# Performance work log

Hardware: AMD Instinct MI355X
Metric: run time of the kernel (lower is better)

The kernel has to match this reference:

```python
import jax, jax.numpy as jnp
import numpy as np

B, IN_UNITS, C, U, K = 32, 16, 8192, 32, 16
NUM_ITERS = 3


def setup_inputs() -> dict:
    key = jax.random.key(0)
    k1, k2 = jax.random.split(key)
    x = jax.random.normal(k1, (B, IN_UNITS, C), dtype=jnp.float32)
    # W corresponds to the torch parameter of shape (1, C, U, K, IN_UNITS), leading 1 dropped
    W = jax.random.normal(k2, (C, U, K, IN_UNITS), dtype=jnp.float32)
    return {"x": x, "W": W}


def reference(x, W):
    batch = x.shape[0]
    # u_hat[b,c,u,k] = sum_i W[c,u,k,i] * x[b,i,c]   (torch: W @ x after transpose/stack)
    u_hat = jnp.einsum('cuki,bic->bcuk', W, x)
    b_ij = jnp.zeros((C, U), dtype=x.dtype)
    v = None
    for _ in range(NUM_ITERS):
        c_ij = jax.nn.softmax(b_ij, axis=0)            # softmax over in_channels (dim=1 in torch)
        s = jnp.einsum('cu,bcuk->buk', c_ij, u_hat)    # weighted sum over channels
        # squash: note the original sums over dim=2 of (B,1,U,K,1) == the num_units axis
        mag_sq = jnp.sum(s ** 2, axis=1, keepdims=True)  # (B,1,K)
        mag = jnp.sqrt(mag_sq)
        v = mag_sq / (1.0 + mag_sq) * (s / mag)          # (B,U,K)
        # agreement: mean over batch of <u_hat, v>
        a = jnp.einsum('bcuk,buk->cu', u_hat, v) / batch
        b_ij = b_ij + a
    return v[..., None]  # matches torch output (B, num_units, unit_size, 1)
```

## Files before the change

kernel.cpp:

```cpp
#include <hip/hip_runtime.h>

#define CC   8192
#define UU   32
#define BB   32
#define INU  16
#define UK   512
#define CPB  32
#define NBLK 256
#define XS_STRIDE 528

template <int CTRL>
__device__ __forceinline__ float dpp_add(float x) {
  int p = __builtin_amdgcn_update_dpp(0, __float_as_int(x), CTRL, 0xF, 0xF, true);
  return x + __int_as_float(p);
}

__global__ __launch_bounds__(512, 2) void fused_pass(
    const float* __restrict__ x, const float* __restrict__ W,
    const float* __restrict__ v_in, float* __restrict__ b_io,
    float* __restrict__ S, float* __restrict__ Z, const int iter0)
{
    __shared__ float xs[16 * XS_STRIDE];

    const int t  = threadIdx.x;
    const int w  = t >> 6;
    const int l  = t & 63;
    const int k  = l & 15;
    const int bg = l >> 4;
    const int u0 = w * 4;
    const int c0 = blockIdx.x * CPB;

    float v[4][8], Sl[4][8];
#pragma unroll
    for (int j = 0; j < 4; ++j)
#pragma unroll
      for (int bb = 0; bb < 8; ++bb) Sl[j][bb] = 0.f;

    if (iter0) {
#pragma unroll
      for (int j = 0; j < 4; ++j)
#pragma unroll
        for (int bb = 0; bb < 8; ++bb) v[j][bb] = 0.f;
    } else {
#pragma unroll
      for (int j = 0; j < 4; ++j)
#pragma unroll
        for (int bb = 0; bb < 8; ++bb)
          v[j][bb] = v_in[(bg * 8 + bb) * UK + (u0 + j) * 16 + k];
    }
    float zloc[4] = {0.f, 0.f, 0.f, 0.f};

    for (int cc = 0; cc < CPB; ++cc) {
        if ((cc & 15) == 0) {
            __syncthreads();
            const int cbase = c0 + (cc & ~15);
#pragma unroll
            for (int jj = 0; jj < 16; ++jj) {
                int idx = jj * 512 + t;
                int ccl = idx & 15;
                int bi  = idx >> 4;
                int b   = bi >> 4, i = bi & 15;
                xs[ccl * XS_STRIDE + (b & 7) * 64 + (b >> 3) * 16 + i] = x[bi * CC + cbase + ccl];
            }
            __syncthreads();
        }

        const int c = c0 + cc;

        float bold[4] = {0.f, 0.f, 0.f, 0.f};
        if (!iter0) {
#pragma unroll
            for (int j = 0; j < 4; ++j) bold[j] = b_io[(size_t)c * UU + u0 + j];
        }

        float4 wq[4][4];
        {
            const float4* wp = (const float4*)(W + ((size_t)c * UK + (size_t)u0 * 16 + k) * INU);
#pragma unroll
            for (int j = 0; j < 4; ++j)
#pragma unroll
                for (int q = 0; q < 4; ++q) wq[j][q] = wp[j * 64 + q];
        }

        float uh[4][8];
        float ap[4] = {0.f, 0.f, 0.f, 0.f};
        const float* xrow = &xs[(cc & 15) * XS_STRIDE + bg * 16];
#pragma unroll
        for (int bb = 0; bb < 8; ++bb) {
            const float4* xr = (const float4*)(xrow + bb * 64);
            float4 x0 = xr[0], x1 = xr[1], x2 = xr[2], x3 = xr[3];
#pragma unroll
            for (int j = 0; j < 4; ++j) {
                float h;
                h = wq[j][0].x * x0.x;
                h = fmaf(wq[j][0].y, x0.y, h); h = fmaf(wq[j][0].z, x0.z, h); h = fmaf(wq[j][0].w, x0.w, h);
                h = fmaf(wq[j][1].x, x1.x, h); h = fmaf(wq[j][1].y, x1.y, h);
                h = fmaf(wq[j][1].z, x1.z, h); h = fmaf(wq[j][1].w, x1.w, h);
                h = fmaf(wq[j][2].x, x2.x, h); h = fmaf(wq[j][2].y, x2.y, h);
                h = fmaf(wq[j][2].z, x2.z, h); h = fmaf(wq[j][2].w, x2.w, h);
                h = fmaf(wq[j][3].x, x3.x, h); h = fmaf(wq[j][3].y, x3.y, h);
                h = fmaf(wq[j][3].z, x3.z, h); h = fmaf(wq[j][3].w, x3.w, h);
                uh[j][bb] = h;
                ap[j] = fmaf(h, v[j][bb], ap[j]);
            }
        }

#pragma unroll
        for (int j = 0; j < 4; ++j) {
            float a = ap[j];
            a = dpp_add<0xB1>(a);
            a = dpp_add<0x4E>(a);
            a = dpp_add<0x141>(a);
            a = dpp_add<0x140>(a);
            a += __shfl_xor(a, 16);
            a += __shfl_xor(a, 32);
            ap[j] = a;
        }

#pragma unroll
        for (int j = 0; j < 4; ++j) {
            float bnew = bold[j] + ap[j] * (1.0f / 32.0f);
            float e = __expf(bnew);
            zloc[j] += e;
            if (l == 0) b_io[(size_t)c * UU + u0 + j] = bnew;
#pragma unroll
            for (int bb = 0; bb < 8; ++bb) Sl[j][bb] = fmaf(e, uh[j][bb], Sl[j][bb]);
        }
    }

#pragma unroll
    for (int j = 0; j < 4; ++j)
#pragma unroll
        for (int bb = 0; bb < 8; ++bb)
            atomicAdd(S + (bg * 8 + bb) * UK + (u0 + j) * 16 + k, Sl[j][bb]);
    if (l == 0) {
#pragma unroll
        for (int j = 0; j < 4; ++j) atomicAdd(Z + u0 + j, zloc[j]);
    }
}

__global__ void squash_k(const float* __restrict__ S, const float* __restrict__ Z,
                         float* __restrict__ vout)
{
    __shared__ float z_sh[UU];
    __shared__ float s2_sh[UK];
    __shared__ float mag_sh[16];

    const int b = blockIdx.x;
    const int t = threadIdx.x;

    if (t < UU) z_sh[t] = Z[t];
    float ssum = S[b * UK + t];
    __syncthreads();

    float s = ssum / z_sh[t >> 4];
    s2_sh[t] = s * s;
    __syncthreads();

    if (t < 16) {
        float m = 0.f;
        for (int uu = 0; uu < UU; ++uu) m += s2_sh[uu * 16 + t];
        mag_sh[t] = m;
    }
    __syncthreads();

    float msq = mag_sh[t & 15];
    float out = (msq / (1.0f + msq)) * s / sqrtf(msq);
    vout[b * UK + t] = out;
}

extern "C" void kernel_launch(void* const* d_in, const int* in_sizes, int n_in,
                              void* d_out, int out_size, void* d_ws, size_t ws_size,
                              hipStream_t stream)
{
    const float* x = (const float*)d_in[0];
    const float* W = (const float*)d_in[1];
    float* out = (float*)d_out;

    char* ws = (char*)d_ws;
    const size_t SLOT = 65536 + 256;
    float* vb  = (float*)(ws + 3 * SLOT);
    float* bio = (float*)(ws + 3 * SLOT + 65536);

    hipMemsetAsync(ws, 0, 3 * SLOT, stream);

    for (int pass = 0; pass < 3; ++pass) {
        float* S = (float*)(ws + pass * SLOT);
        float* Z = (float*)(ws + pass * SLOT + 65536);
        fused_pass<<<NBLK, 512, 0, stream>>>(x, W, vb, bio, S, Z, pass == 0 ? 1 : 0);
        squash_k<<<BB, 512, 0, stream>>>(S, Z, (pass == 2) ? out : vb);
    }
}
```

Baseline: 770.2 us.

## Fuse all routing passes into one cooperative kernel with register-resident logits

Replaces the six launches (three fused passes plus three squash kernels) with a single cooperative kernel that uses grid.sync between passes. Each block recomputes the squash redundantly to get v in registers, and routing logits b stay in registers via readlane instead of a global round trip. Blocks grow to 1024 threads with 2 units per wave, and the channel traversal alternates direction across passes so the most recently loaded W rows may still be cached. The costs are the grid-wide barrier, redundant per-block squash work with shared-memory atomics, and higher register pressure under launch_bounds(1024,4).

```diff
diff --git a/kernel.cpp b/kernel.cpp
--- a/kernel.cpp
+++ b/kernel.cpp
@@ -1,4 +1,7 @@
 #include <hip/hip_runtime.h>
+#include <hip/hip_cooperative_groups.h>
+
+namespace cg = cooperative_groups;
 
 #define CC   8192
 #define UU   32
@@ -7,7 +10,8 @@
 #define UK   512
 #define CPB  32
 #define NBLK 256
-#define XS_STRIDE 528
+#define HALF 16
+#define XSTR 532
 
 template <int CTRL>
 __device__ __forceinline__ float dpp_add(float x) {
@@ -15,179 +19,228 @@
   return x + __int_as_float(p);
 }
 
-__global__ __launch_bounds__(512, 2) void fused_pass(
+__device__ __forceinline__ float red64(float a) {
+  a = dpp_add<0xB1>(a);
+  a = dpp_add<0x4E>(a);
+  a = dpp_add<0x141>(a);
+  a = dpp_add<0x140>(a);
+  a += __shfl_xor(a, 16);
+  a += __shfl_xor(a, 32);
+  return a;
+}
+
+__global__ __launch_bounds__(1024, 4) void caps_all(
     const float* __restrict__ x, const float* __restrict__ W,
-    const float* __restrict__ v_in, float* __restrict__ b_io,
-    float* __restrict__ S, float* __restrict__ Z, const int iter0)
+    float* __restrict__ Sg, float* __restrict__ Zg, float* __restrict__ out)
 {
-    __shared__ float xs[16 * XS_STRIDE];
-
-    const int t  = threadIdx.x;
-    const int w  = t >> 6;
-    const int l  = t & 63;
-    const int k  = l & 15;
-    const int bg = l >> 4;
-    const int u0 = w * 4;
-    const int c0 = blockIdx.x * CPB;
-
-    float v[4][8], Sl[4][8];
-#pragma unroll
-    for (int j = 0; j < 4; ++j)
-#pragma unroll
-      for (int bb = 0; bb < 8; ++bb) Sl[j][bb] = 0.f;
-
-    if (iter0) {
-#pragma unroll
-      for (int j = 0; j < 4; ++j)
-#pragma unroll
-        for (int bb = 0; bb < 8; ++bb) v[j][bb] = 0.f;
-    } else {
-#pragma unroll
-      for (int j = 0; j < 4; ++j)
-#pragma unroll
-        for (int bb = 0; bb < 8; ++bb)
-          v[j][bb] = v_in[(bg * 8 + bb) * UK + (u0 + j) * 16 + k];
+  __shared__ float xs[HALF * XSTR];
+  __shared__ float msq[BB * 16];
+
+  const int t  = threadIdx.x;
+  const int l  = t & 63;
+  const int k  = l & 15;
+  const int bg = l >> 4;
+  const int u0 = (t >> 6) * 2;
+  const int c0 = blockIdx.x * CPB;
+
+  float b0 = 0.f, b1 = 0.f;
+  float v0[8], v1[8];
+#pragma unroll
+  for (int bb = 0; bb < 8; ++bb) { v0[bb] = 0.f; v1[bb] = 0.f; }
+
+  cg::grid_group grid = cg::this_grid();
+
+#pragma unroll 1
+  for (int pass = 0; pass < 3; ++pass) {
+    float* S = Sg + pass * (BB * UK);
+    float* Z = Zg + pass * UU;
+    const int dir = pass & 1;
+
+    float Sl0[8], Sl1[8];
+#pragma unroll
+    for (int bb = 0; bb < 8; ++bb) { Sl0[bb] = 0.f; Sl1[bb] = 0.f; }
+    float z0 = 0.f, z1 = 0.f;
+
+#pragma unroll 1
+    for (int hh = 0; hh < 2; ++hh) {
+      const int h = dir ? (1 - hh) : hh;
+      const int cbase = c0 + h * HALF;
+      __syncthreads();
+#pragma unroll
+      for (int jj = 0; jj < 8; ++jj) {
+        int idx = jj * 1024 + t;
+        int ccl = idx & 15, bi = idx >> 4;
+        int b = bi >> 4, i = bi & 15;
+        xs[ccl * XSTR + (b & 7) * 64 + (b >> 3) * 16 + i] = x[bi * CC + cbase + ccl];
+      }
+      __syncthreads();
+
+#pragma unroll 1
+      for (int ci = 0; ci < HALF; ++ci) {
+        const int ccl = dir ? (HALF - 1 - ci) : ci;
+        const int c   = cbase + ccl;
+        const int cc  = h * HALF + ccl;
+
+        const float4* wp = (const float4*)(W + ((size_t)c * UK + u0 * 16 + k) * INU);
+        float4 wa0 = wp[0],  wa1 = wp[1],  wa2 = wp[2],  wa3 = wp[3];
+        float4 wb0 = wp[64], wb1 = wp[65], wb2 = wp[66], wb3 = wp[67];
+
+        float uh0[8], uh1[8];
+        float ap0 = 0.f, ap1 = 0.f;
+        const float* xr0 = xs + ccl * XSTR + bg * 16;
+#pragma unroll
+        for (int bb = 0; bb < 8; ++bb) {
+          const float4* xr = (const float4*)(xr0 + bb * 64);
+          float4 x0 = xr[0], x1 = xr[1], x2 = xr[2], x3 = xr[3];
+          float h0, h1;
+          h0 = wa0.x * x0.x;
+          h0 = fmaf(wa0.y, x0.y, h0); h0 = fmaf(wa0.z, x0.z, h0); h0 = fmaf(wa0.w, x0.w, h0);
+          h0 = fmaf(wa1.x, x1.x, h0); h0 = fmaf(wa1.y, x1.y, h0);
+          h0 = fmaf(wa1.z, x1.z, h0); h0 = fmaf(wa1.w, x1.w, h0);
+          h0 = fmaf(wa2.x, x2.x, h0); h0 = fmaf(wa2.y, x2.y, h0);
+          h0 = fmaf(wa2.z, x2.z, h0); h0 = fmaf(wa2.w, x2.w, h0);
+          h0 = fmaf(wa3.x, x3.x, h0); h0 = fmaf(wa3.y, x3.y, h0);
+          h0 = fmaf(wa3.z, x3.z, h0); h0 = fmaf(wa3.w, x3.w, h0);
+          h1 = wb0.x * x0.x;
+          h1 = fmaf(wb0.y, x0.y, h1); h1 = fmaf(wb0.z, x0.z, h1); h1 = fmaf(wb0.w, x0.w, h1);
+          h1 = fmaf(wb1.x, x1.x, h1); h1 = fmaf(wb1.y, x1.y, h1);
+          h1 = fmaf(wb1.z, x1.z, h1); h1 = fmaf(wb1.w, x1.w, h1);
+          h1 = fmaf(wb2.x, x2.x, h1); h1 = fmaf(wb2.y, x2.y, h1);
+          h1 = fmaf(wb2.z, x2.z, h1); h1 = fmaf(wb2.w, x2.w, h1);
+          h1 = fmaf(wb3.x, x3.x, h1); h1 = fmaf(wb3.y, x3.y, h1);
+          h1 = fmaf(wb3.z, x3.z, h1); h1 = fmaf(wb3.w, x3.w, h1);
+          uh0[bb] = h0; uh1[bb] = h1;
+          ap0 = fmaf(h0, v0[bb], ap0);
+          ap1 = fmaf(h1, v1[bb], ap1);
+        }
+
+        ap0 = red64(ap0);
+        ap1 = red64(ap1);
+
+        float bo0 = __int_as_float(__builtin_amdgcn_readlane(__float_as_int(b0), cc));
+        float bo1 = __int_as_float(__builtin_amdgcn_readlane(__float_as_int(b1), cc));
+        float bn0 = fmaf(ap0, 0.03125f, bo0);
+        float bn1 = fmaf(ap1, 0.03125f, bo1);
+        b0 = (l == cc) ? bn0 : b0;
+        b1 = (l == cc) ? bn1 : b1;
+        float e0 = __expf(bn0);
+        float e1 = __expf(bn1);
+        z0 += e0; z1 += e1;
+#pragma unroll
+        for (int bb = 0; bb < 8; ++bb) {
+          Sl0[bb] = fmaf(e0, uh0[bb], Sl0[bb]);
+          Sl1[bb] = fmaf(e1, uh1[bb], Sl1[bb]);
+        }
+      }
     }
-    float zloc[4] = {0.f, 0.f, 0.f, 0.f};
-
-    for (int cc = 0; cc < CPB; ++cc) {
-        if ((cc & 15) == 0) {
-            __syncthreads();
-            const int cbase = c0 + (cc & ~15);
-#pragma unroll
-            for (int jj = 0; jj < 16; ++jj) {
-                int idx = jj * 512 + t;
-                int ccl = idx & 15;
-                int bi  = idx >> 4;
-                int b   = bi >> 4, i = bi & 15;
-                xs[ccl * XS_STRIDE + (b & 7) * 64 + (b >> 3) * 16 + i] = x[bi * CC + cbase + ccl];
-            }
-            __syncthreads();
+
+#pragma unroll
+    for (int bb = 0; bb < 8; ++bb) {
+      atomicAdd(S + (bg * 8 + bb) * UK + u0 * 16 + k,       Sl0[bb]);
+      atomicAdd(S + (bg * 8 + bb) * UK + (u0 + 1) * 16 + k, Sl1[bb]);
+    }
+    if (l == 0) { atomicAdd(Z + u0, z0); atomicAdd(Z + u0 + 1, z1); }
+
+    __threadfence();
+    grid.sync();
+
+    if (pass < 2) {
+      if (t < 512) msq[t] = 0.f;
+      __syncthreads();
+      {
+        const int b = t >> 5, uu2 = t & 31;
+        float rz = 1.0f / Z[uu2];
+        const float4* sp = (const float4*)(S + t * 16);
+        float4 s0 = sp[0], s1 = sp[1], s2 = sp[2], s3 = sp[3];
+        float* mrow = msq + b * 16;
+        float q;
+        q = s0.x * rz; atomicAdd(mrow + 0,  q * q);
+        q = s0.y * rz; atomicAdd(mrow + 1,  q * q);
+        q = s0.z * rz; atomicAdd(mrow + 2,  q * q);
+        q = s0.w * rz; atomicAdd(mrow + 3,  q * q);
+        q = s1.x * rz; atomicAdd(mrow + 4,  q * q);
+        q = s1.y * rz; atomicAdd(mrow + 5,  q * q);
+        q = s1.z * rz; atomicAdd(mrow + 6,  q * q);
+        q = s1.w * rz; atomicAdd(mrow + 7,  q * q);
+        q = s2.x * rz; atomicAdd(mrow + 8,  q * q);
+        q = s2.y * rz; atomicAdd(mrow + 9,  q * q);
+        q = s2.z * rz; atomicAdd(mrow + 10, q * q);
+        q = s2.w * rz; atomicAdd(mrow + 11, q * q);
+        q = s3.x * rz; atomicAdd(mrow + 12, q * q);
+        q = s3.y * rz; atomicAdd(mrow + 13, q * q);
+        q = s3.z * rz; atomicAdd(mrow + 14, q * q);
+        q = s3.w * rz; atomicAdd(mrow + 15, q * q);
+      }
+      __syncthreads();
+      {
+        float rz0 = 1.0f / Z[u0], rz1 = 1.0f / Z[u0 + 1];
+#pragma unroll
+        for (int bb = 0; bb < 8; ++bb) {
+          int b = bg * 8 + bb;
+          float m = msq[b * 16 + k];
+          float g = sqrtf(m) / (1.0f + m);
+          v0[bb] = S[b * UK + u0 * 16 + k] * rz0 * g;
+          v1[bb] = S[b * UK + (u0 + 1) * 16 + k] * rz1 * g;
         }
-
-        const int c = c0 + cc;
-
-        float bold[4] = {0.f, 0.f, 0.f, 0.f};
-        if (!iter0) {
-#pragma unroll
-            for (int j = 0; j < 4; ++j) bold[j] = b_io[(size_t)c * UU + u0 + j];
-        }
-
-        float4 wq[4][4];
-        {
-            const float4* wp = (const float4*)(W + ((size_t)c * UK + (size_t)u0 * 16 + k) * INU);
-#pragma unroll
-            for (int j = 0; j < 4; ++j)
-#pragma unroll
-                for (int q = 0; q < 4; ++q) wq[j][q] = wp[j * 64 + q];
-        }
-
-        float uh[4][8];
-        float ap[4] = {0.f, 0.f, 0.f, 0.f};
-        const float* xrow = &xs[(cc & 15) * XS_STRIDE + bg * 16];
-#pragma unroll
-        for (int bb = 0; bb < 8; ++bb) {
-            const float4* xr = (const float4*)(xrow + bb * 64);
-            float4 x0 = xr[0], x1 = xr[1], x2 = xr[2], x3 = xr[3];
-#pragma unroll
-            for (int j = 0; j < 4; ++j) {
-                float h;
-                h = wq[j][0].x * x0.x;
-                h = fmaf(wq[j][0].y, x0.y, h); h = fmaf(wq[j][0].z, x0.z, h); h = fmaf(wq[j][0].w, x0.w, h);
-                h = fmaf(wq[j][1].x, x1.x, h); h = fmaf(wq[j][1].y, x1.y, h);
-                h = fmaf(wq[j][1].z, x1.z, h); h = fmaf(wq[j][1].w, x1.w, h);
-                h = fmaf(wq[j][2].x, x2.x, h); h = fmaf(wq[j][2].y, x2.y, h);
-                h = fmaf(wq[j][2].z, x2.z, h); h = fmaf(wq[j][2].w, x2.w, h);
-                h = fmaf(wq[j][3].x, x3.x, h); h = fmaf(wq[j][3].y, x3.y, h);
-                h = fmaf(wq[j][3].z, x3.z, h); h = fmaf(wq[j][3].w, x3.w, h);
-                uh[j][bb] = h;
-                ap[j] = fmaf(h, v[j][bb], ap[j]);
-            }
-        }
-
-#pragma unroll
-        for (int j = 0; j < 4; ++j) {
-            float a = ap[j];
-            a = dpp_add<0xB1>(a);
-            a = dpp_add<0x4E>(a);
-            a = dpp_add<0x141>(a);
-            a = dpp_add<0x140>(a);
-            a += __shfl_xor(a, 16);
-            a += __shfl_xor(a, 32);
-            ap[j] = a;
-        }
-
-#pragma unroll
-        for (int j = 0; j < 4; ++j) {
-            float bnew = bold[j] + ap[j] * (1.0f / 32.0f);
-            float e = __expf(bnew);
-            zloc[j] += e;
-            if (l == 0) b_io[(size_t)c * UU + u0 + j] = bnew;
-#pragma unroll
-            for (int bb = 0; bb < 8; ++bb) Sl[j][bb] = fmaf(e, uh[j][bb], Sl[j][bb]);
-        }
+      }
+    } else if (blockIdx.x == 0) {
+      if (t < 512) msq[t] = 0.f;
+      __syncthreads();
+      const int b = t >> 5, uu2 = t & 31;
+      float rz = 1.0f / Z[uu2];
+      const float4* sp = (const float4*)(S + t * 16);
+      float4 s0 = sp[0], s1 = sp[1], s2 = sp[2], s3 = sp[3];
+      s0.x *= rz; s0.y *= rz; s0.z *= rz; s0.w *= rz;
+      s1.x *= rz; s1.y *= rz; s1.z *= rz; s1.w *= rz;
+      s2.x *= rz; s2.y *= rz; s2.z *= rz; s2.w *= rz;
+      s3.x *= rz; s3.y *= rz; s3.z *= rz; s3.w *= rz;
+      float* mrow = msq + b * 16;
+      atomicAdd(mrow + 0,  s0.x * s0.x); atomicAdd(mrow + 1,  s0.y * s0.y);
+      atomicAdd(mrow + 2,  s0.z * s0.z); atomicAdd(mrow + 3,  s0.w * s0.w);
+      atomicAdd(mrow + 4,  s1.x * s1.x); atomicAdd(mrow + 5,  s1.y * s1.y);
+      atomicAdd(mrow + 6,  s1.z * s1.z); atomicAdd(mrow + 7,  s1.w * s1.w);
+      atomicAdd(mrow + 8,  s2.x * s2.x); atomicAdd(mrow + 9,  s2.y * s2.y);
+      atomicAdd(mrow + 10, s2.z * s2.z); atomicAdd(mrow + 11, s2.w * s2.w);
+      atomicAdd(mrow + 12, s3.x * s3.x); atomicAdd(mrow + 13, s3.y * s3.y);
+      atomicAdd(mrow + 14, s3.z * s3.z); atomicAdd(mrow + 15, s3.w * s3.w);
+      __syncthreads();
+      float4 o0, o1, o2, o3;
+      o0.x = s0.x * sqrtf(mrow[0])  / (1.0f + mrow[0]);
+      o0.y = s0.y * sqrtf(mrow[1])  / (1.0f + mrow[1]);
+      o0.z = s0.z * sqrtf(mrow[2])  / (1.0f + mrow[2]);
+      o0.w = s0.w * sqrtf(mrow[3])  / (1.0f + mrow[3]);
+      o1.x = s1.x * sqrtf(mrow[4])  / (1.0f + mrow[4]);
+      o1.y = s1.y * sqrtf(mrow[5])  / (1.0f + mrow[5]);
+      o1.z = s1.z * sqrtf(mrow[6])  / (1.0f + mrow[6]);
+      o1.w = s1.w * sqrtf(mrow[7])  / (1.0f + mrow[7]);
+      o2.x = s2.x * sqrtf(mrow[8])  / (1.0f + mrow[8]);
+      o2.y = s2.y * sqrtf(mrow[9])  / (1.0f + mrow[9]);
+      o2.z = s2.z * sqrtf(mrow[10]) / (1.0f + mrow[10]);
+      o2.w = s2.w * sqrtf(mrow[11]) / (1.0f + mrow[11]);
+      o3.x = s3.x * sqrtf(mrow[12]) / (1.0f + mrow[12]);
+      o3.y = s3.y * sqrtf(mrow[13]) / (1.0f + mrow[13]);
+      o3.z = s3.z * sqrtf(mrow[14]) / (1.0f + mrow[14]);
+      o3.w = s3.w * sqrtf(mrow[15]) / (1.0f + mrow[15]);
+      float4* op = (float4*)(out + t * 16);
+      op[0] = o0; op[1] = o1; op[2] = o2; op[3] = o3;
     }
-
-#pragma unroll
-    for (int j = 0; j < 4; ++j)
-#pragma unroll
-        for (int bb = 0; bb < 8; ++bb)
-            atomicAdd(S + (bg * 8 + bb) * UK + (u0 + j) * 16 + k, Sl[j][bb]);
-    if (l == 0) {
-#pragma unroll
-        for (int j = 0; j < 4; ++j) atomicAdd(Z + u0 + j, zloc[j]);
-    }
-}
-
-__global__ void squash_k(const float* __restrict__ S, const float* __restrict__ Z,
-                         float* __restrict__ vout)
-{
-    __shared__ float z_sh[UU];
-    __shared__ float s2_sh[UK];
-    __shared__ float mag_sh[16];
-
-    const int b = blockIdx.x;
-    const int t = threadIdx.x;
-
-    if (t < UU) z_sh[t] = Z[t];
-    float ssum = S[b * UK + t];
-    __syncthreads();
-
-    float s = ssum / z_sh[t >> 4];
-    s2_sh[t] = s * s;
-    __syncthreads();
-
-    if (t < 16) {
-        float m = 0.f;
-        for (int uu = 0; uu < UU; ++uu) m += s2_sh[uu * 16 + t];
-        mag_sh[t] = m;
-    }
-    __syncthreads();
-
-    float msq = mag_sh[t & 15];
-    float out = (msq / (1.0f + msq)) * s / sqrtf(msq);
-    vout[b * UK + t] = out;
+  }
 }
 
 extern "C" void kernel_launch(void* const* d_in, const int* in_sizes, int n_in,
                               void* d_out, int out_size, void* d_ws, size_t ws_size,
                               hipStream_t stream)
 {
-    const float* x = (const float*)d_in[0];
-    const float* W = (const float*)d_in[1];
-    float* out = (float*)d_out;
-
-    char* ws = (char*)d_ws;
-    const size_t SLOT = 65536 + 256;
-    float* vb  = (float*)(ws + 3 * SLOT);
-    float* bio = (float*)(ws + 3 * SLOT + 65536);
-
-    hipMemsetAsync(ws, 0, 3 * SLOT, stream);
-
-    for (int pass = 0; pass < 3; ++pass) {
-        float* S = (float*)(ws + pass * SLOT);
-        float* Z = (float*)(ws + pass * SLOT + 65536);
-        fused_pass<<<NBLK, 512, 0, stream>>>(x, W, vb, bio, S, Z, pass == 0 ? 1 : 0);
-        squash_k<<<BB, 512, 0, stream>>>(S, Z, (pass == 2) ? out : vb);
-    }
-}
+  const float* x = (const float*)d_in[0];
+  const float* W = (const float*)d_in[1];
+  float* out = (float*)d_out;
+
+  float* Sg = (float*)d_ws;
+  float* Zg = (float*)((char*)d_ws + 3 * BB * UK * 4);
+
+  (void)hipMemsetAsync(d_ws, 0, 3 * BB * UK * 4 + 3 * UU * 4, stream);
+
+  void* args[] = { (void*)&x, (void*)&W, (void*)&Sg, (void*)&Zg, (void*)&out };
+  (void)hipLaunchCooperativeKernel(reinterpret_cast<void*>(caps_all),
+                                   dim3(NBLK), dim3(1024), args, 0, stream);
+}
```

New measurement: 1.283 ms. 66.6% more time.

## Fold squash into fused pass, halve chunk size, reverse chunk order per pass

Applied to the files above, without the earlier changes.

Each pass now recomputes the squashed v from the previous pass's S and Z inside every block, which removes two squash kernel launches. CPB drops to 16 with 512 blocks and launch bounds of 4 blocks per SM to raise occupancy. Routing logits are kept in registers and updated with readlane, with one store at the end, and odd passes walk the chunks in reverse so the W and x read last are still in cache. The cost is that every block redundantly reads S_prev and recomputes the magnitudes, and more blocks mean more atomic adds into S.

```diff
diff --git a/kernel.cpp b/kernel.cpp
--- a/kernel.cpp
+++ b/kernel.cpp
@@ -5,9 +5,10 @@
 #define BB   32
 #define INU  16
 #define UK   512
-#define CPB  32
-#define NBLK 256
-#define XS_STRIDE 528
+#define CPB    16
+#define NCHUNK 512
+#define XSTR  532
+#define MSTR  17
 
 template <int CTRL>
 __device__ __forceinline__ float dpp_add(float x) {
@@ -15,179 +16,211 @@
   return x + __int_as_float(p);
 }
 
-__global__ __launch_bounds__(512, 2) void fused_pass(
+__device__ __forceinline__ float red64(float a) {
+  a = dpp_add<0xB1>(a);
+  a = dpp_add<0x4E>(a);
+  a = dpp_add<0x141>(a);
+  a = dpp_add<0x140>(a);
+  a += __shfl_xor(a, 16);
+  a += __shfl_xor(a, 32);
+  return a;
+}
+
+__global__ __launch_bounds__(512, 4) void fused_pass(
     const float* __restrict__ x, const float* __restrict__ W,
-    const float* __restrict__ v_in, float* __restrict__ b_io,
-    float* __restrict__ S, float* __restrict__ Z, const int iter0)
+    float* __restrict__ b_io,
+    const float* __restrict__ S_prev, const float* __restrict__ Z_prev,
+    float* __restrict__ S, float* __restrict__ Z, const int pass)
 {
-    __shared__ float xs[16 * XS_STRIDE];
-
-    const int t  = threadIdx.x;
-    const int w  = t >> 6;
-    const int l  = t & 63;
-    const int k  = l & 15;
-    const int bg = l >> 4;
-    const int u0 = w * 4;
-    const int c0 = blockIdx.x * CPB;
-
-    float v[4][8], Sl[4][8];
+  __shared__ float xs[CPB * XSTR];
+  __shared__ float zr_sh[UU];
+  __shared__ float msq_sh[BB * MSTR];
+
+  const int t  = threadIdx.x;
+  const int l  = t & 63;
+  const int k  = l & 15;
+  const int bg = l >> 4;
+  const int u0 = (t >> 6) * 4;
+  const int dir = pass & 1;
+  const int chunk = dir ? (NCHUNK - 1 - blockIdx.x) : blockIdx.x;
+  const int c0 = chunk * CPB;
+
+  float v[4][8];
+  float breg[4] = {0.f, 0.f, 0.f, 0.f};
+
+  if (pass == 0) {
 #pragma unroll
     for (int j = 0; j < 4; ++j)
 #pragma unroll
-      for (int bb = 0; bb < 8; ++bb) Sl[j][bb] = 0.f;
-
-    if (iter0) {
+      for (int bb = 0; bb < 8; ++bb) v[j][bb] = 0.f;
+  } else {
+#pragma unroll
+    for (int j = 0; j < 4; ++j)
+      breg[j] = b_io[(size_t)(c0 + (l & 15)) * UU + u0 + j];
+
+    if (t < UU) zr_sh[t] = 1.0f / Z_prev[t];
+    __syncthreads();
+    {
+      const int b = t >> 4, k2 = t & 15;
+      float m = 0.f;
+#pragma unroll
+      for (int uu = 0; uu < UU; ++uu) {
+        float s = S_prev[b * UK + uu * 16 + k2] * zr_sh[uu];
+        m = fmaf(s, s, m);
+      }
+      msq_sh[b * MSTR + k2] = m;
+    }
+    __syncthreads();
+    {
+      float zr0 = zr_sh[u0], zr1 = zr_sh[u0 + 1], zr2 = zr_sh[u0 + 2], zr3 = zr_sh[u0 + 3];
+#pragma unroll
+      for (int bb = 0; bb < 8; ++bb) {
+        const int b = bg * 8 + bb;
+        float m = msq_sh[b * MSTR + k];
+        float g = sqrtf(m) / (1.0f + m);
+        v[0][bb] = S_prev[b * UK + (u0 + 0) * 16 + k] * zr0 * g;
+        v[1][bb] = S_prev[b * UK + (u0 + 1) * 16 + k] * zr1 * g;
+        v[2][bb] = S_prev[b * UK + (u0 + 2) * 16 + k] * zr2 * g;
+        v[3][bb] = S_prev[b * UK + (u0 + 3) * 16 + k] * zr3 * g;
+      }
+    }
+    __syncthreads();
+  }
+
+#pragma unroll
+  for (int jj = 0; jj < 16; ++jj) {
+    int idx = jj * 512 + t;
+    int ccl = idx & 15, bi = idx >> 4;
+    int b = bi >> 4, i = bi & 15;
+    xs[ccl * XSTR + (b & 7) * 64 + (b >> 3) * 16 + i] = x[bi * CC + c0 + ccl];
+  }
+  __syncthreads();
+
+  float Sl[4][8];
+#pragma unroll
+  for (int j = 0; j < 4; ++j)
+#pragma unroll
+    for (int bb = 0; bb < 8; ++bb) Sl[j][bb] = 0.f;
+  float zloc[4] = {0.f, 0.f, 0.f, 0.f};
+
+#pragma unroll 1
+  for (int cc = 0; cc < CPB; ++cc) {
+    const int c = c0 + cc;
+
+    float4 wq[4][4];
+    {
+      const float4* wp = (const float4*)(W + ((size_t)c * UK + u0 * 16 + k) * INU);
 #pragma unroll
       for (int j = 0; j < 4; ++j)
 #pragma unroll
-        for (int bb = 0; bb < 8; ++bb) v[j][bb] = 0.f;
-    } else {
-#pragma unroll
-      for (int j = 0; j < 4; ++j)
-#pragma unroll
-        for (int bb = 0; bb < 8; ++bb)
-          v[j][bb] = v_in[(bg * 8 + bb) * UK + (u0 + j) * 16 + k];
-    }
-    float zloc[4] = {0.f, 0.f, 0.f, 0.f};
-
-    for (int cc = 0; cc < CPB; ++cc) {
-        if ((cc & 15) == 0) {
-            __syncthreads();
-            const int cbase = c0 + (cc & ~15);
-#pragma unroll
-            for (int jj = 0; jj < 16; ++jj) {
-                int idx = jj * 512 + t;
-                int ccl = idx & 15;
-                int bi  = idx >> 4;
-                int b   = bi >> 4, i = bi & 15;
-                xs[ccl * XS_STRIDE + (b & 7) * 64 + (b >> 3) * 16 + i] = x[bi * CC + cbase + ccl];
-            }
-            __syncthreads();
-        }
-
-        const int c = c0 + cc;
-
-        float bold[4] = {0.f, 0.f, 0.f, 0.f};
-        if (!iter0) {
-#pragma unroll
-            for (int j = 0; j < 4; ++j) bold[j] = b_io[(size_t)c * UU + u0 + j];
-        }
-
-        float4 wq[4][4];
-        {
-            const float4* wp = (const float4*)(W + ((size_t)c * UK + (size_t)u0 * 16 + k) * INU);
-#pragma unroll
-            for (int j = 0; j < 4; ++j)
-#pragma unroll
-                for (int q = 0; q < 4; ++q) wq[j][q] = wp[j * 64 + q];
-        }
-
-        float uh[4][8];
-        float ap[4] = {0.f, 0.f, 0.f, 0.f};
-        const float* xrow = &xs[(cc & 15) * XS_STRIDE + bg * 16];
-#pragma unroll
-        for (int bb = 0; bb < 8; ++bb) {
-            const float4* xr = (const float4*)(xrow + bb * 64);
-            float4 x0 = xr[0], x1 = xr[1], x2 = xr[2], x3 = xr[3];
-#pragma unroll
-            for (int j = 0; j < 4; ++j) {
-                float h;
-                h = wq[j][0].x * x0.x;
-                h = fmaf(wq[j][0].y, x0.y, h); h = fmaf(wq[j][0].z, x0.z, h); h = fmaf(wq[j][0].w, x0.w, h);
-                h = fmaf(wq[j][1].x, x1.x, h); h = fmaf(wq[j][1].y, x1.y, h);
-                h = fmaf(wq[j][1].z, x1.z, h); h = fmaf(wq[j][1].w, x1.w, h);
-                h = fmaf(wq[j][2].x, x2.x, h); h = fmaf(wq[j][2].y, x2.y, h);
-                h = fmaf(wq[j][2].z, x2.z, h); h = fmaf(wq[j][2].w, x2.w, h);
-                h = fmaf(wq[j][3].x, x3.x, h); h = fmaf(wq[j][3].y, x3.y, h);
-                h = fmaf(wq[j][3].z, x3.z, h); h = fmaf(wq[j][3].w, x3.w, h);
-                uh[j][bb] = h;
-                ap[j] = fmaf(h, v[j][bb], ap[j]);
-            }
-        }
-
-#pragma unroll
-        for (int j = 0; j < 4; ++j) {
-            float a = ap[j];
-            a = dpp_add<0xB1>(a);
-            a = dpp_add<0x4E>(a);
-            a = dpp_add<0x141>(a);
-            a = dpp_add<0x140>(a);
-            a += __shfl_xor(a, 16);
-            a += __shfl_xor(a, 32);
-            ap[j] = a;
-        }
-
-#pragma unroll
-        for (int j = 0; j < 4; ++j) {
-            float bnew = bold[j] + ap[j] * (1.0f / 32.0f);
-            float e = __expf(bnew);
-            zloc[j] += e;
-            if (l == 0) b_io[(size_t)c * UU + u0 + j] = bnew;
-#pragma unroll
-            for (int bb = 0; bb < 8; ++bb) Sl[j][bb] = fmaf(e, uh[j][bb], Sl[j][bb]);
-        }
-    }
-
+        for (int q = 0; q < 4; ++q) wq[j][q] = wp[j * 64 + q];
+    }
+
+    float uh[4][8];
+    float ap[4] = {0.f, 0.f, 0.f, 0.f};
+    const float* xr0 = xs + cc * XSTR + bg * 16;
+#pragma unroll
+    for (int bb = 0; bb < 8; ++bb) {
+      const float4* xr = (const float4*)(xr0 + bb * 64);
+      float4 x0 = xr[0], x1 = xr[1], x2 = xr[2], x3 = xr[3];
+#pragma unroll
+      for (int j = 0; j < 4; ++j) {
+        float h;
+        h = wq[j][0].x * x0.x;
+        h = fmaf(wq[j][0].y, x0.y, h); h = fmaf(wq[j][0].z, x0.z, h); h = fmaf(wq[j][0].w, x0.w, h);
+        h = fmaf(wq[j][1].x, x1.x, h); h = fmaf(wq[j][1].y, x1.y, h);
+        h = fmaf(wq[j][1].z, x1.z, h); h = fmaf(wq[j][1].w, x1.w, h);
+        h = fmaf(wq[j][2].x, x2.x, h); h = fmaf(wq[j][2].y, x2.y, h);
+        h = fmaf(wq[j][2].z, x2.z, h); h = fmaf(wq[j][2].w, x2.w, h);
+        h = fmaf(wq[j][3].x, x3.x, h); h = fmaf(wq[j][3].y, x3.y, h);
+        h = fmaf(wq[j][3].z, x3.z, h); h = fmaf(wq[j][3].w, x3.w, h);
+        uh[j][bb] = h;
+        ap[j] = fmaf(h, v[j][bb], ap[j]);
+      }
+    }
+
+#pragma unroll
+    for (int j = 0; j < 4; ++j) ap[j] = red64(ap[j]);
+
+#pragma unroll
+    for (int j = 0; j < 4; ++j) {
+      float bo = __int_as_float(__builtin_amdgcn_readlane(__float_as_int(breg[j]), cc));
+      float bn = fmaf(ap[j], 0.03125f, bo);
+      breg[j] = (l == cc) ? bn : breg[j];
+      float e = __expf(bn);
+      zloc[j] += e;
+#pragma unroll
+      for (int bb = 0; bb < 8; ++bb) Sl[j][bb] = fmaf(e, uh[j][bb], Sl[j][bb]);
+    }
+  }
+
+#pragma unroll
+  for (int j = 0; j < 4; ++j)
+#pragma unroll
+    for (int bb = 0; bb < 8; ++bb)
+      atomicAdd(S + (bg * 8 + bb) * UK + (u0 + j) * 16 + k, Sl[j][bb]);
+  if (l == 0) {
+#pragma unroll
+    for (int j = 0; j < 4; ++j) atomicAdd(Z + u0 + j, zloc[j]);
+  }
+  if (pass < 2 && l < 16) {
 #pragma unroll
     for (int j = 0; j < 4; ++j)
-#pragma unroll
-        for (int bb = 0; bb < 8; ++bb)
-            atomicAdd(S + (bg * 8 + bb) * UK + (u0 + j) * 16 + k, Sl[j][bb]);
-    if (l == 0) {
-#pragma unroll
-        for (int j = 0; j < 4; ++j) atomicAdd(Z + u0 + j, zloc[j]);
-    }
+      b_io[(size_t)(c0 + l) * UU + u0 + j] = breg[j];
+  }
 }
 
 __global__ void squash_k(const float* __restrict__ S, const float* __restrict__ Z,
                          float* __restrict__ vout)
 {
-    __shared__ float z_sh[UU];
-    __shared__ float s2_sh[UK];
-    __shared__ float mag_sh[16];
-
-    const int b = blockIdx.x;
-    const int t = threadIdx.x;
-
-    if (t < UU) z_sh[t] = Z[t];
-    float ssum = S[b * UK + t];
-    __syncthreads();
-
-    float s = ssum / z_sh[t >> 4];
-    s2_sh[t] = s * s;
-    __syncthreads();
-
-    if (t < 16) {
-        float m = 0.f;
-        for (int uu = 0; uu < UU; ++uu) m += s2_sh[uu * 16 + t];
-        mag_sh[t] = m;
-    }
-    __syncthreads();
-
-    float msq = mag_sh[t & 15];
-    float out = (msq / (1.0f + msq)) * s / sqrtf(msq);
-    vout[b * UK + t] = out;
+  __shared__ float z_sh[UU];
+  __shared__ float s2_sh[UK];
+  __shared__ float mag_sh[16];
+
+  const int b = blockIdx.x;
+  const int t = threadIdx.x;
+
+  if (t < UU) z_sh[t] = Z[t];
+  float ssum = S[b * UK + t];
+  __syncthreads();
+
+  float s = ssum / z_sh[t >> 4];
+  s2_sh[t] = s * s;
+  __syncthreads();
+
+  if (t < 16) {
+    float m = 0.f;
+    for (int uu = 0; uu < UU; ++uu) m += s2_sh[uu * 16 + t];
+    mag_sh[t] = m;
+  }
+  __syncthreads();
+
+  float msq = mag_sh[t & 15];
+  vout[b * UK + t] = (msq / (1.0f + msq)) * s / sqrtf(msq);
 }
 
 extern "C" void kernel_launch(void* const* d_in, const int* in_sizes, int n_in,
                               void* d_out, int out_size, void* d_ws, size_t ws_size,
                               hipStream_t stream)
 {
-    const float* x = (const float*)d_in[0];
-    const float* W = (const float*)d_in[1];
-    float* out = (float*)d_out;
-
-    char* ws = (char*)d_ws;
-    const size_t SLOT = 65536 + 256;
-    float* vb  = (float*)(ws + 3 * SLOT);
-    float* bio = (float*)(ws + 3 * SLOT + 65536);
-
-    hipMemsetAsync(ws, 0, 3 * SLOT, stream);
-
-    for (int pass = 0; pass < 3; ++pass) {
-        float* S = (float*)(ws + pass * SLOT);
-        float* Z = (float*)(ws + pass * SLOT + 65536);
-        fused_pass<<<NBLK, 512, 0, stream>>>(x, W, vb, bio, S, Z, pass == 0 ? 1 : 0);
-        squash_k<<<BB, 512, 0, stream>>>(S, Z, (pass == 2) ? out : vb);
-    }
-}
+  const float* x = (const float*)d_in[0];
+  const float* W = (const float*)d_in[1];
+  float* out = (float*)d_out;
+
+  char* ws = (char*)d_ws;
+  const size_t SSLOT = (size_t)BB * UK * 4;
+  float* Sg  = (float*)ws;
+  float* Zg  = (float*)(ws + 3 * SSLOT);
+  float* bio = (float*)(ws + 3 * SSLOT + 512);
+
+  (void)hipMemsetAsync(ws, 0, 3 * SSLOT + 512, stream);
+
+  for (int pass = 0; pass < 3; ++pass) {
+    float* S  = Sg + pass * (BB * UK);
+    float* Z  = Zg + pass * UU;
+    const float* Sp = (pass > 0) ? (Sg + (pass - 1) * (BB * UK)) : Sg;
+    const float* Zp = (pass > 0) ? (Zg + (pass - 1) * UU) : Zg;
+    fused_pass<<<NCHUNK, 512, 0, stream>>>(x, W, bio, Sp, Zp, S, Z, pass);
+  }
+  squash_k<<<BB, 512, 0, stream>>>(Sg + 2 * (BB * UK), Zg + 2 * UU, out);
+}
```

Result: slower. 1.527 ms (+98.3%).
